# Performance work log

Hardware: AMD Instinct MI355X
Metric: run time of the kernel (lower is better)

## Reference

```python
import jax, jax.numpy as jnp
import numpy as np

N_NODES = 100000
N_EDGES = 1600000
B = 16
NMAX = 4096
IN_DIM = 32
H1 = 64      # capacity C
H2 = 128     # 2C
LAT = 64
DEC_H = 128  # 2C
DEC_IN = LAT + 2
FUEL = 5


def _ln(x, g, b):
    m = x.mean(-1, keepdims=True)
    v = x.var(-1, keepdims=True)
    return (x - m) / jnp.sqrt(v + 1e-5) * g + b


def _mlp2(x, wi, bi, g, be, wo, bo):
    # DeepMLP with num_layers=2: in_lin -> LayerNorm -> ReLU -> out_lin
    h = jax.nn.relu(_ln(x @ wi + bi, g, be))
    return h @ wo + bo


def setup_inputs() -> dict:
    key = jax.random.key(0)
    ks = jax.random.split(key, 48)
    d = {}
    d['x'] = jax.random.normal(ks[0], (N_NODES, IN_DIM), jnp.float32)
    d['edge_index'] = jax.random.randint(ks[1], (2, N_EDGES), 0, N_NODES)
    d['batch'] = jnp.sort(jax.random.randint(ks[2], (N_NODES,), 0, B))

    def w(k, shape):
        return (jax.random.normal(k, shape, jnp.float32) * 0.02)

    conv_shapes = {'w1m': (IN_DIM, H1), 'w2m': (H1, H2), 'w3m': (H2, LAT),
                   'w1l': (IN_DIM, H1), 'w2l': (H1, H2), 'w3l': (H2, LAT)}
    i = 3
    for nm, sh in conv_shapes.items():
        d[nm] = w(ks[i], sh); i += 1
        d['b' + nm[1:]] = jnp.zeros((sh[1],), jnp.float32)
    # node_mlp (DeepMLP dec_in->dec_h->dec_h)
    d['nm_wi'] = w(ks[i], (DEC_IN, DEC_H)); i += 1
    d['nm_bi'] = jnp.zeros((DEC_H,), jnp.float32)
    d['nm_g'] = jnp.ones((DEC_H,), jnp.float32)
    d['nm_be'] = jnp.zeros((DEC_H,), jnp.float32)
    d['nm_wo'] = w(ks[i], (DEC_H, DEC_H)); i += 1
    d['nm_bo'] = jnp.zeros((DEC_H,), jnp.float32)
    # heads
    d['ex_w'] = w(ks[i], (DEC_H, 1)); i += 1
    d['ex_b'] = jnp.zeros((1,), jnp.float32)
    d['fu_w'] = w(ks[i], (DEC_H, FUEL)); i += 1
    d['fu_b'] = jnp.zeros((FUEL,), jnp.float32)
    d['al_w'] = w(ks[i], (DEC_H, 1)); i += 1
    d['al_b'] = jnp.zeros((1,), jnp.float32)
    d['sl_w'] = w(ks[i], (DEC_H, 1)); i += 1
    d['sl_b'] = jnp.zeros((1,), jnp.float32)
    # edge_mlp (DeepMLP dec_in->dec_h->8)
    d['em_wi'] = w(ks[i], (DEC_IN, DEC_H)); i += 1
    d['em_bi'] = jnp.zeros((DEC_H,), jnp.float32)
    d['em_g'] = jnp.ones((DEC_H,), jnp.float32)
    d['em_be'] = jnp.zeros((DEC_H,), jnp.float32)
    d['em_wo'] = w(ks[i], (DEC_H, 8)); i += 1
    d['em_bo'] = jnp.zeros((8,), jnp.float32)
    d['pos_all'] = jax.random.normal(ks[i], (NMAX, 2), jnp.float32)
    return d


def reference(x, edge_index, batch,
              w1m, b1m, w2m, b2m, w3m, b3m,
              w1l, b1l, w2l, b2l, w3l, b3l,
              nm_wi, nm_bi, nm_g, nm_be, nm_wo, nm_bo,
              ex_w, ex_b, fu_w, fu_b, al_w, al_b, sl_w, sl_b,
              em_wi, em_bi, em_g, em_be, em_wo, em_bo,
              pos_all):
    # ---- GCN encoder with self-loops and symmetric normalization (PyG GCNConv) ----
    loops = jnp.arange(N_NODES)
    src = jnp.concatenate([edge_index[0], loops])
    dst = jnp.concatenate([edge_index[1], loops])
    deg = jax.ops.segment_sum(jnp.ones(src.shape, jnp.float32), dst, N_NODES)
    dinv = jax.lax.rsqrt(deg)  # deg >= 1 because of self-loops
    norm = (dinv[src] * dinv[dst])[:, None]

    def conv(h, wt, bt):
        hw = h @ wt                                   # [N, F_out]
        return jax.ops.segment_sum(norm * hw[src], dst, N_NODES) + bt

    mu = jax.nn.relu(conv(x, w1m, b1m))
    mu = jax.nn.relu(conv(mu, w2m, b2m))
    mu = jax.nn.relu(conv(mu, w3m, b3m))
    lg = jax.nn.relu(conv(x, w1l, b1l))
    lg = jax.nn.relu(conv(lg, w2l, b2l))
    lg = jax.nn.relu(conv(lg, w3l, b3l))

    cnt = jnp.maximum(jax.ops.segment_sum(jnp.ones((N_NODES,), jnp.float32), batch, B), 1.0)[:, None]
    mu_g = jax.ops.segment_sum(mu, batch, B) / cnt    # global_mean_pool [B, LAT]
    lg_g = jax.ops.segment_sum(lg, batch, B) / cnt

    z = mu_g  # eval-mode latent_sample returns mu

    # ---- decoder ----
    Z = jnp.broadcast_to(z[:, None, :], (B, NMAX, LAT))
    pos = jnp.broadcast_to(pos_all[None], (B, NMAX, 2))
    Zp = jnp.concatenate([Z, pos], -1).reshape(B * NMAX, DEC_IN)
    h = _mlp2(Zp, nm_wi, nm_bi, nm_g, nm_be, nm_wo, nm_bo)
    nodes = (h @ ex_w + ex_b).reshape(B, NMAX, 1)
    fuel = (h @ fu_w + fu_b).reshape(B, NMAX, FUEL)
    alt = (h @ al_w + al_b).reshape(B, NMAX, 1)
    slope = (h @ sl_w + sl_b).reshape(B, NMAX, 1)
    edges = _mlp2(Zp, em_wi, em_bi, em_g, em_be, em_wo, em_bo).reshape(B, NMAX, 8)
    return (nodes, edges, fuel, alt, slope, mu_g, lg_g)
```

## Files before the change

### kernel.cpp

```cpp
#include <hip/hip_runtime.h>
#include <hip/hip_bf16.h>

#define N_NODES 100000
#define N_EDGESC 1600000
#define BATCH_B 16
#define NMAXC 4096
#define LATC 64
#define NBINS 391
#define NSB 256
#define EPB ((N_EDGESC + NSB - 1) / NSB)
#define BIN_PAD 768

#define OUT_NODES 0
#define OUT_EDGES 65536
#define OUT_FUEL  589824
#define OUT_ALT   917504
#define OUT_SLOPE 983040
#define OUT_MU    1048576
#define OUT_LG    1049600

typedef float f32x2 __attribute__((ext_vector_type(2)));
typedef float f32x4 __attribute__((ext_vector_type(4)));
typedef short bf16x8 __attribute__((ext_vector_type(8)));
union U4B { uint4 u; bf16x8 b; };

__device__ __forceinline__ unsigned short f2bf(float f) {
    unsigned int u = __float_as_uint(f);
    return (unsigned short)((u + 0x7FFFu + ((u >> 16) & 1u)) >> 16);
}
__device__ __forceinline__ float bf2f(unsigned short h) {
    return __uint_as_float(((unsigned int)h) << 16);
}
__device__ __forceinline__ void f8acc(unsigned int u, float& a0, float& a1, float& a2, float& a3) {
    f32x2 lo = __builtin_amdgcn_cvt_pk_f32_fp8(u, false);
    f32x2 hi = __builtin_amdgcn_cvt_pk_f32_fp8(u, true);
    a0 += lo[0]; a1 += lo[1]; a2 += hi[0]; a3 += hi[1];
}
__device__ __forceinline__ void f8_to_bf2(unsigned int u, unsigned int& q0, unsigned int& q1) {
    f32x2 lo = __builtin_amdgcn_cvt_pk_f32_fp8(u, false);
    f32x2 hi = __builtin_amdgcn_cvt_pk_f32_fp8(u, true);
    q0 = (unsigned int)f2bf(lo[0]) | ((unsigned int)f2bf(lo[1]) << 16);
    q1 = (unsigned int)f2bf(hi[0]) | ((unsigned int)f2bf(hi[1]) << 16);
}

__global__ __launch_bounds__(1024) void histA(const int* __restrict__ dst, int* __restrict__ hist) {
    __shared__ int h[NBINS];
    int b = blockIdx.x, t = threadIdx.x;
    for (int i = t; i < NBINS; i += 1024) h[i] = 0;
    __syncthreads();
    int e0 = b * EPB, e1 = min(e0 + EPB, N_EDGESC);
    for (int i = e0 + t; i < e1; i += 1024)
        atomicAdd(&h[dst[i] >> 8], 1);
    __syncthreads();
    for (int i = t; i < NBINS; i += 1024) hist[i * NSB + b] = h[i];
}

__global__ void scanB(int* __restrict__ hist, int* __restrict__ total) {
    __shared__ int sh[NSB];
    int j = blockIdx.x, t = threadIdx.x;
    int v = hist[j * NSB + t];
    sh[t] = v; __syncthreads();
    for (int off = 1; off < NSB; off <<= 1) {
        int u = (t >= off) ? sh[t - off] : 0; __syncthreads();
        sh[t] += u; __syncthreads();
    }
    hist[j * NSB + t] = sh[t] - v;
    if (t == NSB - 1) total[j] = sh[t];
}

__global__ void scanC(const int* __restrict__ total, int* __restrict__ base) {
    __shared__ int sh[512];
    int t = threadIdx.x;
    int v = (t < NBINS) ? total[t] : 0;
    sh[t] = v; __syncthreads();
    for (int off = 1; off < 512; off <<= 1) {
        int u = (t >= off) ? sh[t - off] : 0; __syncthreads();
        sh[t] += u; __syncthreads();
    }
    if (t < NBINS) base[t] = sh[t] - v;
    if (t == NBINS - 1) base[NBINS] = sh[t];
}

__global__ __launch_bounds__(1024) void scatterD(const int* __restrict__ src, const int* __restrict__ dst,
                                                 const int* __restrict__ hist, const int* __restrict__ base,
                                                 unsigned int* __restrict__ sorted) {
    __shared__ int w0[NBINS];
    __shared__ int lc[NBINS];
    int b = blockIdx.x, t = threadIdx.x;
    for (int i = t; i < NBINS; i += 1024) {
        w0[i] = base[i] + hist[i * NSB + b];
        lc[i] = 0;
    }
    __syncthreads();
    int e0 = b * EPB, e1 = min(e0 + EPB, N_EDGESC);
    for (int i = e0 + t; i < e1; i += 1024) {
        int d = dst[i], s = src[i];
        int j = d >> 8;
        int r = atomicAdd(&lc[j], 1);
        sorted[w0[j] + r] = ((unsigned int)s << 8) | (d & 255);
    }
}

__global__ void csr_compact(const unsigned int* __restrict__ sorted, const int* __restrict__ base,
                            const float* __restrict__ x,
                            int* __restrict__ adj, int* __restrict__ offs,
                            int* __restrict__ cnt, float* __restrict__ dinv,
                            unsigned int* __restrict__ xs8, int N) {
    __shared__ int lc[256];
    __shared__ int cur[256];
    __shared__ int so4[256];
    int j = blockIdx.x, t = threadIdx.x;
    lc[t] = 0; cur[t] = 0;
    __syncthreads();
    int e0 = base[j], e1 = base[j + 1];
    for (int i = e0 + t; i < e1; i += 256)
        atomicAdd(&lc[sorted[i] & 255], 1);
    __syncthreads();
    int c4 = (lc[t] + 3) & ~3;
    so4[t] = c4;
    __syncthreads();
    for (int off = 1; off < 256; off <<= 1) {
        int u = (t >= off) ? so4[t - off] : 0; __syncthreads();
        so4[t] += u; __syncthreads();
    }
    int mybase = base[j] + j * BIN_PAD + so4[t] - c4;
    __syncthreads();
    so4[t] = mybase;
    __syncthreads();
    for (int i = e0 + t; i < e1; i += 256) {
        unsigned int pk = sorted[i];
        int d = pk & 255;
        int r = atomicAdd(&cur[d], 1);
        adj[so4[d] + r] = (int)(pk >> 8);
    }
    int n = j * 256 + t;
    if (n < N) {
        int c = lc[t];
        cnt[n] = c;
        offs[n] = so4[t];
        float dv = rsqrtf((float)(c + 1));
        dinv[n] = dv;
        float ds = dv * 64.f;
        const float* xr = &x[(size_t)n * 32];
        unsigned int q[8];
#pragma unroll
        for (int jj = 0; jj < 8; jj++) {
            float4 v = *(const float4*)&xr[jj * 4];
            unsigned int r8 = 0;
            r8 = __builtin_amdgcn_cvt_pk_fp8_f32(v.x * ds, v.y * ds, r8, false);
            r8 = __builtin_amdgcn_cvt_pk_fp8_f32(v.z * ds, v.w * ds, r8, true);
            q[jj] = r8;
        }
        *(uint4*)&xs8[(size_t)n * 8] = make_uint4(q[0], q[1], q[2], q[3]);
        *(uint4*)&xs8[(size_t)n * 8 + 4] = make_uint4(q[4], q[5], q[6], q[7]);
    }
}

__global__ void agg_s32(const unsigned int* __restrict__ xs8, const int* __restrict__ cnt,
                        const int* __restrict__ offs, const int* __restrict__ adj,
                        const float* __restrict__ dinv, unsigned short* __restrict__ outb, int N) {
    int t = threadIdx.x;
    int sub = t >> 3, f = t & 7;
    int n = blockIdx.x * 32 + sub;
    if (n >= N) return;
    float s0 = 0.f, s1 = 0.f, s2 = 0.f, s3 = 0.f;
    f8acc(xs8[(size_t)n * 8 + f], s0, s1, s2, s3);
    int e = offs[n];
    int e1 = e + cnt[n];
    for (; e + 8 <= e1; e += 8) {
        int4 ia = *(const int4*)&adj[e];
        int4 ib = *(const int4*)&adj[e + 4];
        unsigned int u0 = xs8[(size_t)ia.x * 8 + f];
        unsigned int u1 = xs8[(size_t)ia.y * 8 + f];
        unsigned int u2 = xs8[(size_t)ia.z * 8 + f];
        unsigned int u3 = xs8[(size_t)ia.w * 8 + f];
        unsigned int u4 = xs8[(size_t)ib.x * 8 + f];
        unsigned int u5 = xs8[(size_t)ib.y * 8 + f];
        unsigned int u6 = xs8[(size_t)ib.z * 8 + f];
        unsigned int u7 = xs8[(size_t)ib.w * 8 + f];
        f8acc(u0, s0, s1, s2, s3); f8acc(u1, s0, s1, s2, s3);
        f8acc(u2, s0, s1, s2, s3); f8acc(u3, s0, s1, s2, s3);
        f8acc(u4, s0, s1, s2, s3); f8acc(u5, s0, s1, s2, s3);
        f8acc(u6, s0, s1, s2, s3); f8acc(u7, s0, s1, s2, s3);
    }
    if (e + 4 <= e1) {
        int4 ia = *(const int4*)&adj[e];
        unsigned int u0 = xs8[(size_t)ia.x * 8 + f];
        unsigned int u1 = xs8[(size_t)ia.y * 8 + f];
        unsigned int u2 = xs8[(size_t)ia.z * 8 + f];
        unsigned int u3 = xs8[(size_t)ia.w * 8 + f];
        f8acc(u0, s0, s1, s2, s3); f8acc(u1, s0, s1, s2, s3);
        f8acc(u2, s0, s1, s2, s3); f8acc(u3, s0, s1, s2, s3);
        e += 4;
    }
    for (; e < e1; e++) f8acc(xs8[(size_t)adj[e] * 8 + f], s0, s1, s2, s3);
    float d = dinv[n] * (1.f / 64.f);
    ushort4 o;
    o.x = f2bf(s0 * d); o.y = f2bf(s1 * d); o.z = f2bf(s2 * d); o.w = f2bf(s3 * d);
    *(ushort4*)&outb[(size_t)n * 32 + f * 4] = o;
}

template <bool BIASRELU, bool OUT8>
__global__ void agg128(const unsigned int* __restrict__ tbl, const int* __restrict__ cnt,
                       const int* __restrict__ offs, const int* __restrict__ adj,
                       const float* __restrict__ dinv, const float* __restrict__ bias,
                       void* __restrict__ outv, int N) {
    int t = threadIdx.x;
    int sub = t >> 5, f = t & 31;
    int n = blockIdx.x * 8 + sub;
    if (n >= N) return;
    float s0 = 0.f, s1 = 0.f, s2 = 0.f, s3 = 0.f;
    f8acc(tbl[(size_t)n * 32 + f], s0, s1, s2, s3);
    int e = offs[n];
    int e1 = e + cnt[n];
    for (; e + 8 <= e1; e += 8) {
        int4 ia = *(const int4*)&adj[e];
        int4 ib = *(const int4*)&adj[e + 4];
        unsigned int u0 = tbl[(size_t)ia.x * 32 + f];
        unsigned int u1 = tbl[(size_t)ia.y * 32 + f];
        unsigned int u2 = tbl[(size_t)ia.z * 32 + f];
        unsigned int u3 = tbl[(size_t)ia.w * 32 + f];
        unsigned int u4 = tbl[(size_t)ib.x * 32 + f];
        unsigned int u5 = tbl[(size_t)ib.y * 32 + f];
        unsigned int u6 = tbl[(size_t)ib.z * 32 + f];
        unsigned int u7 = tbl[(size_t)ib.w * 32 + f];
        f8acc(u0, s0, s1, s2, s3); f8acc(u1, s0, s1, s2, s3);
        f8acc(u2, s0, s1, s2, s3); f8acc(u3, s0, s1, s2, s3);
        f8acc(u4, s0, s1, s2, s3); f8acc(u5, s0, s1, s2, s3);
        f8acc(u6, s0, s1, s2, s3); f8acc(u7, s0, s1, s2, s3);
    }
    if (e + 4 <= e1) {
        int4 ia = *(const int4*)&adj[e];
        unsigned int u0 = tbl[(size_t)ia.x * 32 + f];
        unsigned int u1 = tbl[(size_t)ia.y * 32 + f];
        unsigned int u2 = tbl[(size_t)ia.z * 32 + f];
        unsigned int u3 = tbl[(size_t)ia.w * 32 + f];
        f8acc(u0, s0, s1, s2, s3); f8acc(u1, s0, s1, s2, s3);
        f8acc(u2, s0, s1, s2, s3); f8acc(u3, s0, s1, s2, s3);
        e += 4;
    }
    for (; e < e1; e++) f8acc(tbl[(size_t)adj[e] * 32 + f], s0, s1, s2, s3);
    float d = dinv[n] * (1.f / 32.f);
    float v0 = s0 * d, v1 = s1 * d, v2 = s2 * d, v3 = s3 * d;
    if (BIASRELU) {
        float4 bv = *(const float4*)&bias[4 * f];
        v0 = fmaxf(v0 + bv.x, 0.f); v1 = fmaxf(v1 + bv.y, 0.f);
        v2 = fmaxf(v2 + bv.z, 0.f); v3 = fmaxf(v3 + bv.w, 0.f);
    }
    if (OUT8) {
        unsigned int r = 0;
        r = __builtin_amdgcn_cvt_pk_fp8_f32(v0 * 32.f, v1 * 32.f, r, false);
        r = __builtin_amdgcn_cvt_pk_fp8_f32(v2 * 32.f, v3 * 32.f, r, true);
        ((unsigned int*)outv)[(size_t)n * 32 + f] = r;
    } else {
        ushort4 u;
        u.x = f2bf(v0); u.y = f2bf(v1); u.z = f2bf(v2); u.w = f2bf(v3);
        *(ushort4*)&((unsigned short*)outv)[(size_t)n * 128 + 4 * f] = u;
    }
}

__device__ __forceinline__ void wfrag_write(const float* W, int F, int col, int k0,
                                            unsigned int* dst) {
    unsigned int q[4];
#pragma unroll
    for (int jj = 0; jj < 4; jj++) {
        float lo = W[(size_t)(k0 + 2 * jj) * F + col];
        float hi = W[(size_t)(k0 + 2 * jj + 1) * F + col];
        q[jj] = (unsigned int)f2bf(lo) | ((unsigned int)f2bf(hi) << 16);
    }
    *(uint4*)dst = make_uint4(q[0], q[1], q[2], q[3]);
}

__global__ void mega_prep(const int* __restrict__ batch,
                          const float* __restrict__ w1m, const float* __restrict__ w1l,
                          const float* __restrict__ b1m, const float* __restrict__ b1l,
                          const float* __restrict__ b3m, const float* __restrict__ b3l,
                          const float* __restrict__ w2m, const float* __restrict__ w2l,
                          const float* __restrict__ w3m, const float* __restrict__ w3l,
                          const float* __restrict__ nm_wo, const float* __restrict__ nm_bo,
                          const float* __restrict__ ex_w, const float* __restrict__ ex_b,
                          const float* __restrict__ fu_w, const float* __restrict__ fu_b,
                          const float* __restrict__ al_w, const float* __restrict__ al_b,
                          const float* __restrict__ sl_w, const float* __restrict__ sl_b,
                          const float* __restrict__ em_wo,
                          int* __restrict__ bcnt, float* __restrict__ bcat1,
                          float* __restrict__ bcat3, float* __restrict__ wtn,
                          float* __restrict__ bcn, float* __restrict__ wte,
                          unsigned int* __restrict__ wf1, unsigned int* __restrict__ wf2,
                          unsigned int* __restrict__ wf3) {
    int blk = blockIdx.x, t = threadIdx.x;
    if (blk == 0) {
        if (t < 128) bcat1[t] = (t < 64) ? b1m[t] : b1l[t - 64];
        else { int f = t - 128; bcat3[f] = (f < 64) ? b3m[f] : b3l[f - 64]; }
        if (t < BATCH_B) {
            int b = t;
            int lo = 0, hi = N_NODES;
            while (lo < hi) { int mid = (lo + hi) >> 1; if (batch[mid] < b) lo = mid + 1; else hi = mid; }
            int start = lo;
            lo = 0; hi = N_NODES;
            while (lo < hi) { int mid = (lo + hi) >> 1; if (batch[mid] <= b) lo = mid + 1; else hi = mid; }
            bcnt[b] = lo - start;
        }
    } else if (blk <= 9) {
        int idx = (blk - 1) * 256 + t;
        if (idx < 1024) {
            int j = idx >> 7, k = idx & 127;
            float s = 0.f;
            for (int m = 0; m < 128; m++) {
                float w = (j == 0) ? ex_w[m] : (j <= 5) ? fu_w[m * 5 + (j - 1)]
                         : (j == 6) ? al_w[m] : sl_w[m];
                s += nm_wo[k * 128 + m] * w;
            }
            wtn[j * 128 + k] = s;
        } else if (idx < 2048) {
            int i2 = idx - 1024;
            int j = i2 >> 7, k = i2 & 127;
            wte[j * 128 + k] = em_wo[k * 8 + j];
        } else if (idx < 2056) {
            int j = idx - 2048;
            float s = (j == 0) ? ex_b[0] : (j <= 5) ? fu_b[j - 1] : (j == 6) ? al_b[0] : sl_b[0];
            for (int m = 0; m < 128; m++) {
                float w = (j == 0) ? ex_w[m] : (j <= 5) ? fu_w[m * 5 + (j - 1)]
                         : (j == 6) ? al_w[m] : sl_w[m];
                s += nm_bo[m] * w;
            }
            bcn[j] = s;
        }
    } else if (blk <= 17) {
        if (t < 64) {
            int c = blk - 10;
            int col = c * 16 + (t & 15);
            int k0 = (t >> 4) * 8;
            unsigned int q[4];
#pragma unroll
            for (int jj = 0; jj < 4; jj++) {
                int ka = k0 + 2 * jj, kb = ka + 1;
                float lo = (col < 64) ? w1m[ka * 64 + col] : w1l[ka * 64 + col - 64];
                float hi = (col < 64) ? w1m[kb * 64 + col] : w1l[kb * 64 + col - 64];
                q[jj] = (unsigned int)f2bf(lo) | ((unsigned int)f2bf(hi) << 16);
            }
            *(uint4*)&wf1[((size_t)c * 64 + t) * 4] = make_uint4(q[0], q[1], q[2], q[3]);
        }
    } else if (blk <= 49) {
        if (t < 64) {
            int bc = blk - 18;
            int c = bc % 8, s = (bc / 8) % 2, y = bc / 16;
            const float* W = y ? w2l : w2m;
            wfrag_write(W, 128, c * 16 + (t & 15), s * 32 + (t >> 4) * 8,
                        &wf2[((size_t)bc * 64 + t) * 4]);
        }
    } else {
        if (t < 64) {
            int bc = blk - 50;
            int c = bc % 4, s = (bc / 4) % 4, y = bc / 16;
            const float* W = y ? w3l : w3m;
            wfrag_write(W, 64, c * 16 + (t & 15), s * 32 + (t >> 4) * 8,
                        &wf3[((size_t)bc * 64 + t) * 4]);
        }
    }
}

__global__ __launch_bounds__(256) void mfma_conv1(
    const unsigned short* __restrict__ inv, const unsigned int* __restrict__ wfrag,
    const float* __restrict__ bias, const float* __restrict__ dinv,
    unsigned int* __restrict__ outv, int N) {
    constexpr int C = 8;
    constexpr int FP = 132;
    __shared__ unsigned short buf[4][16][FP];
    int t = threadIdx.x, lane = t & 63, wave = t >> 6;
    int n0 = blockIdx.x * 64 + wave * 16;

    f32x4 acc[C];
#pragma unroll
    for (int c = 0; c < C; c++) acc[c] = (f32x4)(0.f);

    int arow = n0 + (lane & 15);
    bool aok = arow < N;
    U4B af; af.u = make_uint4(0u, 0u, 0u, 0u);
    if (aok)
        af.u = *(const uint4*)(inv + (size_t)arow * 32 + (lane >> 4) * 8);
#pragma unroll
    for (int c = 0; c < C; c++) {
        U4B wb;
        wb.u = *(const uint4*)&wfrag[((size_t)c * 64 + lane) * 4];
        acc[c] = __builtin_amdgcn_mfma_f32_16x16x32_bf16(af.b, wb.b, acc[c], 0, 0, 0);
    }

#pragma unroll
    for (int c = 0; c < C; c++) {
        int col = c * 16 + (lane & 15);
        float bv = bias[col];
#pragma unroll
        for (int r = 0; r < 4; r++) {
            int row = (lane >> 4) * 4 + r;
            int n = n0 + row;
            float v = fmaxf(acc[c][r] + bv, 0.f) * dinv[min(n, N - 1)];
            buf[wave][row][col] = f2bf(v);
        }
    }
    __syncthreads();

    for (int i = t; i < 64 * 16; i += 256) {
        int row = i / 16;
        int f0 = (i % 16) * 8;
        int n = blockIdx.x * 64 + row;
        if (n >= N) continue;
        const unsigned short* bp = &buf[row >> 4][row & 15][f0];
        uint2 a = *(const uint2*)bp;
        uint2 b = *(const uint2*)(bp + 4);
        float e0 = __uint_as_float(a.x << 16), e1 = __uint_as_float(a.x & 0xFFFF0000u);
        float e2 = __uint_as_float(a.y << 16), e3 = __uint_as_float(a.y & 0xFFFF0000u);
        float e4 = __uint_as_float(b.x << 16), e5 = __uint_as_float(b.x & 0xFFFF0000u);
        float e6 = __uint_as_float(b.y << 16), e7 = __uint_as_float(b.y & 0xFFFF0000u);
        unsigned int r0 = 0, r1 = 0;
        r0 = __builtin_amdgcn_cvt_pk_fp8_f32(e0 * 32.f, e1 * 32.f, r0, false);
        r0 = __builtin_amdgcn_cvt_pk_fp8_f32(e2 * 32.f, e3 * 32.f, r0, true);
        r1 = __builtin_amdgcn_cvt_pk_fp8_f32(e4 * 32.f, e5 * 32.f, r1, false);
        r1 = __builtin_amdgcn_cvt_pk_fp8_f32(e6 * 32.f, e7 * 32.f, r1, true);
        *(uint2*)((unsigned char*)outv + (size_t)n * 128 + f0) = make_uint2(r0, r1);
    }
}

__global__ __launch_bounds__(256) void conv23(
    const unsigned int* __restrict__ hB8, const unsigned int* __restrict__ wf2,
    const unsigned int* __restrict__ wf3, const float* __restrict__ b2m,
    const float* __restrict__ b2l, const float* __restrict__ dinv,
    unsigned int* __restrict__ hD8, int N) {
    __shared__ unsigned short hbuf[4][16][136];
    __shared__ unsigned short obuf[4][16][72];
    int t = threadIdx.x, lane = t & 63, wave = t >> 6;
    int y = blockIdx.y;
    int n0 = blockIdx.x * 64 + wave * 16;
    const float* bias = y ? b2l : b2m;
    const unsigned int* w2 = wf2 + (size_t)y * 2 * 8 * 64 * 4;
    const unsigned int* w3 = wf3 + (size_t)y * 4 * 4 * 64 * 4;

    f32x4 acc2[8];
#pragma unroll
    for (int c = 0; c < 8; c++) acc2[c] = (f32x4)(0.f);
    int arow = n0 + (lane & 15);
    bool aok = arow < N;
#pragma unroll
    for (int s = 0; s < 2; s++) {
        U4B af; af.u = make_uint4(0u, 0u, 0u, 0u);
        if (aok) {
            uint2 u = *(const uint2*)((const unsigned char*)hB8 +
                        (size_t)arow * 128 + y * 64 + s * 32 + (lane >> 4) * 8);
            f8_to_bf2(u.x, af.u.x, af.u.y);
            f8_to_bf2(u.y, af.u.z, af.u.w);
        }
#pragma unroll
        for (int c = 0; c < 8; c++) {
            U4B wb;
            wb.u = *(const uint4*)&w2[((size_t)(s * 8 + c) * 64 + lane) * 4];
            acc2[c] = __builtin_amdgcn_mfma_f32_16x16x32_bf16(af.b, wb.b, acc2[c], 0, 0, 0);
        }
    }
#pragma unroll
    for (int c = 0; c < 8; c++) {
        int col = c * 16 + (lane & 15);
        float bv = bias[col];
#pragma unroll
        for (int r = 0; r < 4; r++) {
            int row = (lane >> 4) * 4 + r;
            float v = fmaxf(acc2[c][r] * (1.f / 32.f) + bv, 0.f);
            hbuf[wave][row][col] = f2bf(v);
        }
    }

    f32x4 acc3[4];
#pragma unroll
    for (int c = 0; c < 4; c++) acc3[c] = (f32x4)(0.f);
#pragma unroll
    for (int s = 0; s < 4; s++) {
        U4B af;
        af.u = *(const uint4*)&hbuf[wave][lane & 15][s * 32 + (lane >> 4) * 8];
#pragma unroll
        for (int c = 0; c < 4; c++) {
            U4B wb;
            wb.u = *(const uint4*)&w3[((size_t)(s * 4 + c) * 64 + lane) * 4];
            acc3[c] = __builtin_amdgcn_mfma_f32_16x16x32_bf16(af.b, wb.b, acc3[c], 0, 0, 0);
        }
    }
#pragma unroll
    for (int c = 0; c < 4; c++) {
        int col = c * 16 + (lane & 15);
#pragma unroll
        for (int r = 0; r < 4; r++) {
            int row = (lane >> 4) * 4 + r;
            int n = n0 + row;
            float v = acc3[c][r] * dinv[min(n, N - 1)];
            obuf[wave][row][col] = f2bf(v);
        }
    }
    __syncthreads();
    for (int i = t; i < 64 * 8; i += 256) {
        int row = i / 8;
        int f0 = (i % 8) * 8;
        int n = blockIdx.x * 64 + row;
        if (n >= N) continue;
        const unsigned short* bp = &obuf[row >> 4][row & 15][f0];
        uint2 a = *(const uint2*)bp;
        uint2 b = *(const uint2*)(bp + 4);
        float e0 = __uint_as_float(a.x << 16), e1 = __uint_as_float(a.x & 0xFFFF0000u);
        float e2 = __uint_as_float(a.y << 16), e3 = __uint_as_float(a.y & 0xFFFF0000u);
        float e4 = __uint_as_float(b.x << 16), e5 = __uint_as_float(b.x & 0xFFFF0000u);
        float e6 = __uint_as_float(b.y << 16), e7 = __uint_as_float(b.y & 0xFFFF0000u);
        unsigned int r0 = 0, r1 = 0;
        r0 = __builtin_amdgcn_cvt_pk_fp8_f32(e0 * 32.f, e1 * 32.f, r0, false);
        r0 = __builtin_amdgcn_cvt_pk_fp8_f32(e2 * 32.f, e3 * 32.f, r0, true);
        r1 = __builtin_amdgcn_cvt_pk_fp8_f32(e4 * 32.f, e5 * 32.f, r1, false);
        r1 = __builtin_amdgcn_cvt_pk_fp8_f32(e6 * 32.f, e7 * 32.f, r1, true);
        *(uint2*)((unsigned char*)hD8 + (size_t)n * 128 + y * 64 + f0) = make_uint2(r0, r1);
    }
}

__global__ __launch_bounds__(256) void pool128(const unsigned int* __restrict__ h,
                                               const int* __restrict__ batch,
                                               float* __restrict__ sums, int n) {
    int t = threadIdx.x, lane = t & 63, wave = t >> 6;
    int r0 = blockIdx.x * 64 + wave * 16;
    if (r0 >= n) return;
    int r1 = min(r0 + 16, n);
    int cur = batch[r0];
    float a0 = 0.f, a1 = 0.f;
    for (int i = r0; i < r1; i++) {
        int b = batch[i];
        if (b != cur) {
            atomicAdd(&sums[cur * 128 + 2 * lane], a0);
            atomicAdd(&sums[cur * 128 + 2 * lane + 1], a1);
            a0 = a1 = 0.f; cur = b;
        }
        unsigned int u = h[(size_t)i * 64 + lane];
        a0 += __uint_as_float(u << 16);
        a1 += __uint_as_float(u & 0xFFFF0000u);
    }
    atomicAdd(&sums[cur * 128 + 2 * lane], a0);
    atomicAdd(&sums[cur * 128 + 2 * lane + 1], a1);
}

__global__ void finalize_zwi(const float* __restrict__ sums, const int* __restrict__ bcnt,
                             const float* __restrict__ nm_wi, const float* __restrict__ nm_bi,
                             const float* __restrict__ em_wi, const float* __restrict__ em_bi,
                             float* __restrict__ out, float* __restrict__ zwi_nm,
                             float* __restrict__ zwi_em) {
    __shared__ float zs[64];
    int b = blockIdx.x, t = threadIdx.x;
    float c = fmaxf((float)bcnt[b], 1.f);
    float v = sums[b * 128 + t] / c;
    if (t < 64) { out[OUT_MU + b * 64 + t] = v; zs[t] = v; }
    else out[OUT_LG + b * 64 + (t - 64)] = v;
    __syncthreads();
    float an = nm_bi[t], ae = em_bi[t];
    for (int k = 0; k < 64; k++) {
        float zv = zs[k];
        an += zv * nm_wi[k * 128 + t];
        ae += zv * em_wi[k * 128 + t];
    }
    zwi_nm[b * 128 + t] = an;
    zwi_em[b * 128 + t] = ae;
}

#define D3_ROWS 32

__global__ __launch_bounds__(256) void decoder3(
    const float* __restrict__ zwi_nm, const float* __restrict__ zwi_em,
    const float* __restrict__ nm_wi, const float* __restrict__ em_wi,
    const float* __restrict__ nm_g, const float* __restrict__ nm_be,
    const float* __restrict__ em_g, const float* __restrict__ em_be,
    const float* __restrict__ wtn, const float* __restrict__ bcn,
    const float* __restrict__ wte, const float* __restrict__ em_bo,
    const float* __restrict__ pos_all,
    float* __restrict__ out) {
    __shared__ float sn[D3_ROWS][132];
    __shared__ float se[D3_ROWS][132];
    __shared__ float Wn[8][132];
    __shared__ float We[8][132];
    int t = threadIdx.x;
    int lane = t & 63, wave = t >> 6;
    int rowBase = blockIdx.x * D3_ROWS;
    int b = rowBase >> 12;
    int row0 = rowBase + wave * 8;

    for (int i = t; i < 1024; i += 256) {
        Wn[i >> 7][i & 127] = wtn[i];
        We[i >> 7][i & 127] = wte[i];
    }

    int f0 = lane, f1 = lane + 64;
    float zn0 = zwi_nm[b * 128 + f0], zn1 = zwi_nm[b * 128 + f1];
    float ze0 = zwi_em[b * 128 + f0], ze1 = zwi_em[b * 128 + f1];
    float wn64_0 = nm_wi[64 * 128 + f0], wn64_1 = nm_wi[64 * 128 + f1];
    float wn65_0 = nm_wi[65 * 128 + f0], wn65_1 = nm_wi[65 * 128 + f1];
    float we64_0 = em_wi[64 * 128 + f0], we64_1 = em_wi[64 * 128 + f1];
    float we65_0 = em_wi[65 * 128 + f0], we65_1 = em_wi[65 * 128 + f1];
    float gn0 = nm_g[f0], gn1 = nm_g[f1], bn0 = nm_be[f0], bn1 = nm_be[f1];
    float ge0 = em_g[f0], ge1 = em_g[f1], be0 = em_be[f0], be1 = em_be[f1];

#pragma unroll
    for (int r = 0; r < 8; r++) {
        int row = row0 + r, i = row & (NMAXC - 1);
        float px = pos_all[i * 2], py = pos_all[i * 2 + 1];
        float a0 = zn0 + px * wn64_0 + py * wn65_0;
        float a1 = zn1 + px * wn64_1 + py * wn65_1;
        float e0 = ze0 + px * we64_0 + py * we65_0;
        float e1 = ze1 + px * we64_1 + py * we65_1;
        float sm = a0 + a1, sq = a0 * a0 + a1 * a1;
        float sme = e0 + e1, sqe = e0 * e0 + e1 * e1;
#pragma unroll
        for (int d = 1; d < 64; d <<= 1) {
            sm += __shfl_xor(sm, d); sq += __shfl_xor(sq, d);
            sme += __shfl_xor(sme, d); sqe += __shfl_xor(sqe, d);
        }
        float mean = sm * (1.f / 128.f);
        float var = sq * (1.f / 128.f) - mean * mean;
        float rstd = rsqrtf(var + 1e-5f);
        int rl = wave * 8 + r;
        sn[rl][f0] = fmaxf((a0 - mean) * rstd * gn0 + bn0, 0.f);
        sn[rl][f1] = fmaxf((a1 - mean) * rstd * gn1 + bn1, 0.f);
        float meane = sme * (1.f / 128.f);
        float vare = sqe * (1.f / 128.f) - meane * meane;
        float rstde = rsqrtf(vare + 1e-5f);
        se[rl][f0] = fmaxf((e0 - meane) * rstde * ge0 + be0, 0.f);
        se[rl][f1] = fmaxf((e1 - meane) * rstde * ge1 + be1, 0.f);
    }
    __syncthreads();

    int rl = t >> 3, j = t & 7;
    float accn = 0.f, acce = 0.f;
#pragma unroll 8
    for (int k4 = 0; k4 < 128; k4 += 4) {
        float4 sv = *(const float4*)&sn[rl][k4];
        float4 wv = *(const float4*)&Wn[j][k4];
        float4 sev = *(const float4*)&se[rl][k4];
        float4 wev = *(const float4*)&We[j][k4];
        accn += sv.x * wv.x + sv.y * wv.y + sv.z * wv.z + sv.w * wv.w;
        acce += sev.x * wev.x + sev.y * wev.y + sev.z * wev.z + sev.w * wev.w;
    }
    int row = rowBase + rl;
    accn += bcn[j];
    if (j == 0)       out[OUT_NODES + row] = accn;
    else if (j <= 5)  out[OUT_FUEL + (size_t)row * 5 + (j - 1)] = accn;
    else if (j == 6)  out[OUT_ALT + row] = accn;
    else              out[OUT_SLOPE + row] = accn;
    out[OUT_EDGES + (size_t)row * 8 + j] = acce + em_bo[j];
}

extern "C" void kernel_launch(void* const* d_in, const int* in_sizes, int n_in,
                              void* d_out, int out_size, void* d_ws, size_t ws_size,
                              hipStream_t stream) {
    const float* x    = (const float*)d_in[0];
    const int* edge   = (const int*)d_in[1];
    const int* batch  = (const int*)d_in[2];
    const float* w1m = (const float*)d_in[3];  const float* b1m = (const float*)d_in[4];
    const float* w2m = (const float*)d_in[5];  const float* b2m = (const float*)d_in[6];
    const float* w3m = (const float*)d_in[7];  const float* b3m = (const float*)d_in[8];
    const float* w1l = (const float*)d_in[9];  const float* b1l = (const float*)d_in[10];
    const float* w2l = (const float*)d_in[11]; const float* b2l = (const float*)d_in[12];
    const float* w3l = (const float*)d_in[13]; const float* b3l = (const float*)d_in[14];
    const float* nm_wi = (const float*)d_in[15]; const float* nm_bi = (const float*)d_in[16];
    const float* nm_g  = (const float*)d_in[17]; const float* nm_be = (const float*)d_in[18];
    const float* nm_wo = (const float*)d_in[19]; const float* nm_bo = (const float*)d_in[20];
    const float* ex_w = (const float*)d_in[21]; const float* ex_b = (const float*)d_in[22];
    const float* fu_w = (const float*)d_in[23]; const float* fu_b = (const float*)d_in[24];
    const float* al_w = (const float*)d_in[25]; const float* al_b = (const float*)d_in[26];
    const float* sl_w = (const float*)d_in[27]; const float* sl_b = (const float*)d_in[28];
    const float* em_wi = (const float*)d_in[29]; const float* em_bi = (const float*)d_in[30];
    const float* em_g  = (const float*)d_in[31]; const float* em_be = (const float*)d_in[32];
    const float* em_wo = (const float*)d_in[33]; const float* em_bo = (const float*)d_in[34];
    const float* pos_all = (const float*)d_in[35];
    float* out = (float*)d_out;

    char* p = (char*)d_ws;
    auto alloc = [&](size_t bytes) -> void* {
        void* r = (void*)p;
        p += ((bytes + 255) / 256) * 256;
        return r;
    };
    int* cnt      = (int*)alloc((size_t)N_NODES * 4);
    int* offs     = (int*)alloc((size_t)N_NODES * 4);
    float* dinv   = (float*)alloc((size_t)N_NODES * 4);
    int* bcnt     = (int*)alloc(BATCH_B * 4);
    float* sums   = (float*)alloc(BATCH_B * 128 * 4);
    float* zwi_nm = (float*)alloc(BATCH_B * 128 * 4);
    float* zwi_em = (float*)alloc(BATCH_B * 128 * 4);
    float* bcat1  = (float*)alloc(128 * 4);
    float* bcat3  = (float*)alloc(128 * 4);
    float* wtn    = (float*)alloc(8 * 128 * 4);
    float* bcn    = (float*)alloc(8 * 4);
    float* wte    = (float*)alloc(8 * 128 * 4);
    unsigned int* wf1 = (unsigned int*)alloc((size_t)8 * 64 * 4 * 4);
    unsigned int* wf2 = (unsigned int*)alloc((size_t)32 * 64 * 4 * 4);
    unsigned int* wf3 = (unsigned int*)alloc((size_t)32 * 64 * 4 * 4);
    int* hist     = (int*)alloc((size_t)NBINS * NSB * 4);
    int* total    = (int*)alloc((size_t)NBINS * 4);
    int* base     = (int*)alloc((size_t)(NBINS + 1) * 4);
    unsigned int* sorted = (unsigned int*)alloc((size_t)N_EDGESC * 4);
    int* adj      = (int*)alloc((size_t)(N_EDGESC + NBINS * BIN_PAD + 256) * 4);
    unsigned int* xs8 = (unsigned int*)alloc((size_t)N_NODES * 8 * 4);
    unsigned short* agg0b = (unsigned short*)alloc((size_t)N_NODES * 32 * 2);
    unsigned int* hA8 = (unsigned int*)alloc((size_t)N_NODES * 32 * 4);
    unsigned int* hB8 = (unsigned int*)alloc((size_t)N_NODES * 32 * 4);
    unsigned short* final128 = (unsigned short*)alloc((size_t)N_NODES * 128 * 2);
    unsigned int* hD8 = hA8;

    const int* srcp = edge;
    const int* dstp = edge + N_EDGESC;

    hipMemsetAsync(sums, 0, (size_t)BATCH_B * 128 * 4, stream);

    mega_prep<<<82, 256, 0, stream>>>(batch, w1m, w1l, b1m, b1l, b3m, b3l,
                                      w2m, w2l, w3m, w3l, nm_wo, nm_bo,
                                      ex_w, ex_b, fu_w, fu_b, al_w, al_b, sl_w, sl_b,
                                      em_wo, bcnt, bcat1, bcat3, wtn, bcn, wte,
                                      wf1, wf2, wf3);

    histA<<<NSB, 1024, 0, stream>>>(dstp, hist);
    scanB<<<NBINS, NSB, 0, stream>>>(hist, total);
    scanC<<<1, 512, 0, stream>>>(total, base);
    scatterD<<<NSB, 1024, 0, stream>>>(srcp, dstp, hist, base, sorted);
    csr_compact<<<NBINS, 256, 0, stream>>>(sorted, base, x, adj, offs, cnt, dinv, xs8, N_NODES);

    agg_s32<<<(N_NODES + 31) / 32, 256, 0, stream>>>(xs8, cnt, offs, adj, dinv, agg0b, N_NODES);

    const int GB = (N_NODES + 63) / 64;

    mfma_conv1<<<GB, 256, 0, stream>>>(agg0b, wf1, bcat1, dinv, hA8, N_NODES);

    agg128<false, true><<<(N_NODES + 7) / 8, 256, 0, stream>>>(
        hA8, cnt, offs, adj, dinv, nullptr, hB8, N_NODES);

    conv23<<<dim3(GB, 2), 256, 0, stream>>>(hB8, wf2, wf3, b2m, b2l, dinv, hD8, N_NODES);

    agg128<true, false><<<(N_NODES + 7) / 8, 256, 0, stream>>>(
        hD8, cnt, offs, adj, dinv, bcat3, final128, N_NODES);

    pool128<<<GB, 256, 0, stream>>>((const unsigned int*)final128, batch, sums, N_NODES);
    finalize_zwi<<<BATCH_B, 128, 0, stream>>>(sums, bcnt, nm_wi, nm_bi, em_wi, em_bi,
                                              out, zwi_nm, zwi_em);

    decoder3<<<BATCH_B * NMAXC / D3_ROWS, 256, 0, stream>>>(
        zwi_nm, zwi_em, nm_wi, em_wi, nm_g, nm_be, em_g, em_be,
        wtn, bcn, wte, em_bo, pos_all, out);
}
```

Before: 259.4 us.

## Slice 128-wide fp8 feature tables into XCD-affine 32-feature planes for aggregation

Stores the fp8 hidden tables as four planar slices of 32 features per node instead of interleaved 128-byte rows. Each aggregation block is mapped, via blockIdx modulo 8, so that a pair of XCDs handles one feature slice, so each XCD's L2 only needs to cache a quarter of the gather table. Producers (conv1, conv23) and the consumer conv23 read are updated for the new layout. The cost is that each thread now gathers 4 bytes from 8 lanes per row, so row reads are shorter, and adjacency and offsets are re-read four times.

```diff
diff --git a/kernel.cpp b/kernel.cpp
--- a/kernel.cpp
+++ b/kernel.cpp
@@ -201,29 +201,34 @@
 }
 
 template <bool BIASRELU, bool OUT8>
-__global__ void agg128(const unsigned int* __restrict__ tbl, const int* __restrict__ cnt,
-                       const int* __restrict__ offs, const int* __restrict__ adj,
-                       const float* __restrict__ dinv, const float* __restrict__ bias,
-                       void* __restrict__ outv, int N) {
+__global__ __launch_bounds__(256) void agg128s(
+    const unsigned int* __restrict__ tbl, const int* __restrict__ cnt,
+    const int* __restrict__ offs, const int* __restrict__ adj,
+    const float* __restrict__ dinv, const float* __restrict__ bias,
+    void* __restrict__ outv, int N) {
     int t = threadIdx.x;
-    int sub = t >> 5, f = t & 31;
-    int n = blockIdx.x * 8 + sub;
+    int sub = t >> 3, f = t & 7;
+    int xcd = blockIdx.x & 7;
+    int slice = xcd >> 1;
+    int chunk = (blockIdx.x >> 3) * 2 + (xcd & 1);
+    int n = chunk * 32 + sub;
     if (n >= N) return;
+    const unsigned int* ts = tbl + (size_t)slice * N * 8;
     float s0 = 0.f, s1 = 0.f, s2 = 0.f, s3 = 0.f;
-    f8acc(tbl[(size_t)n * 32 + f], s0, s1, s2, s3);
+    f8acc(ts[(size_t)n * 8 + f], s0, s1, s2, s3);
     int e = offs[n];
     int e1 = e + cnt[n];
     for (; e + 8 <= e1; e += 8) {
         int4 ia = *(const int4*)&adj[e];
         int4 ib = *(const int4*)&adj[e + 4];
-        unsigned int u0 = tbl[(size_t)ia.x * 32 + f];
-        unsigned int u1 = tbl[(size_t)ia.y * 32 + f];
-        unsigned int u2 = tbl[(size_t)ia.z * 32 + f];
-        unsigned int u3 = tbl[(size_t)ia.w * 32 + f];
-        unsigned int u4 = tbl[(size_t)ib.x * 32 + f];
-        unsigned int u5 = tbl[(size_t)ib.y * 32 + f];
-        unsigned int u6 = tbl[(size_t)ib.z * 32 + f];
-        unsigned int u7 = tbl[(size_t)ib.w * 32 + f];
+        unsigned int u0 = ts[(size_t)ia.x * 8 + f];
+        unsigned int u1 = ts[(size_t)ia.y * 8 + f];
+        unsigned int u2 = ts[(size_t)ia.z * 8 + f];
+        unsigned int u3 = ts[(size_t)ia.w * 8 + f];
+        unsigned int u4 = ts[(size_t)ib.x * 8 + f];
+        unsigned int u5 = ts[(size_t)ib.y * 8 + f];
+        unsigned int u6 = ts[(size_t)ib.z * 8 + f];
+        unsigned int u7 = ts[(size_t)ib.w * 8 + f];
         f8acc(u0, s0, s1, s2, s3); f8acc(u1, s0, s1, s2, s3);
         f8acc(u2, s0, s1, s2, s3); f8acc(u3, s0, s1, s2, s3);
         f8acc(u4, s0, s1, s2, s3); f8acc(u5, s0, s1, s2, s3);
@@ -231,19 +236,19 @@
     }
     if (e + 4 <= e1) {
         int4 ia = *(const int4*)&adj[e];
-        unsigned int u0 = tbl[(size_t)ia.x * 32 + f];
-        unsigned int u1 = tbl[(size_t)ia.y * 32 + f];
-        unsigned int u2 = tbl[(size_t)ia.z * 32 + f];
-        unsigned int u3 = tbl[(size_t)ia.w * 32 + f];
+        unsigned int u0 = ts[(size_t)ia.x * 8 + f];
+        unsigned int u1 = ts[(size_t)ia.y * 8 + f];
+        unsigned int u2 = ts[(size_t)ia.z * 8 + f];
+        unsigned int u3 = ts[(size_t)ia.w * 8 + f];
         f8acc(u0, s0, s1, s2, s3); f8acc(u1, s0, s1, s2, s3);
         f8acc(u2, s0, s1, s2, s3); f8acc(u3, s0, s1, s2, s3);
         e += 4;
     }
-    for (; e < e1; e++) f8acc(tbl[(size_t)adj[e] * 32 + f], s0, s1, s2, s3);
+    for (; e < e1; e++) f8acc(ts[(size_t)adj[e] * 8 + f], s0, s1, s2, s3);
     float d = dinv[n] * (1.f / 32.f);
     float v0 = s0 * d, v1 = s1 * d, v2 = s2 * d, v3 = s3 * d;
     if (BIASRELU) {
-        float4 bv = *(const float4*)&bias[4 * f];
+        float4 bv = ((const float4*)bias)[slice * 8 + f];
         v0 = fmaxf(v0 + bv.x, 0.f); v1 = fmaxf(v1 + bv.y, 0.f);
         v2 = fmaxf(v2 + bv.z, 0.f); v3 = fmaxf(v3 + bv.w, 0.f);
     }
@@ -251,11 +256,11 @@
         unsigned int r = 0;
         r = __builtin_amdgcn_cvt_pk_fp8_f32(v0 * 32.f, v1 * 32.f, r, false);
         r = __builtin_amdgcn_cvt_pk_fp8_f32(v2 * 32.f, v3 * 32.f, r, true);
-        ((unsigned int*)outv)[(size_t)n * 32 + f] = r;
+        ((unsigned int*)outv)[((size_t)slice * N + n) * 8 + f] = r;
     } else {
         ushort4 u;
         u.x = f2bf(v0); u.y = f2bf(v1); u.z = f2bf(v2); u.w = f2bf(v3);
-        *(ushort4*)&((unsigned short*)outv)[(size_t)n * 128 + 4 * f] = u;
+        *(ushort4*)&((unsigned short*)outv)[(size_t)n * 128 + slice * 32 + f * 4] = u;
     }
 }
 
@@ -417,7 +422,8 @@
         r0 = __builtin_amdgcn_cvt_pk_fp8_f32(e2 * 32.f, e3 * 32.f, r0, true);
         r1 = __builtin_amdgcn_cvt_pk_fp8_f32(e4 * 32.f, e5 * 32.f, r1, false);
         r1 = __builtin_amdgcn_cvt_pk_fp8_f32(e6 * 32.f, e7 * 32.f, r1, true);
-        *(uint2*)((unsigned char*)outv + (size_t)n * 128 + f0) = make_uint2(r0, r1);
+        *(uint2*)((unsigned char*)outv + ((size_t)(f0 >> 5) * N + n) * 32 + (f0 & 31))
+            = make_uint2(r0, r1);
     }
 }
 
@@ -445,7 +451,7 @@
         U4B af; af.u = make_uint4(0u, 0u, 0u, 0u);
         if (aok) {
             uint2 u = *(const uint2*)((const unsigned char*)hB8 +
-                        (size_t)arow * 128 + y * 64 + s * 32 + (lane >> 4) * 8);
+                        ((size_t)(y * 2 + s) * N + arow) * 32 + (lane >> 4) * 8);
             f8_to_bf2(u.x, af.u.x, af.u.y);
             f8_to_bf2(u.y, af.u.z, af.u.w);
         }
@@ -511,7 +517,9 @@
         r0 = __builtin_amdgcn_cvt_pk_fp8_f32(e2 * 32.f, e3 * 32.f, r0, true);
         r1 = __builtin_amdgcn_cvt_pk_fp8_f32(e4 * 32.f, e5 * 32.f, r1, false);
         r1 = __builtin_amdgcn_cvt_pk_fp8_f32(e6 * 32.f, e7 * 32.f, r1, true);
-        *(uint2*)((unsigned char*)hD8 + (size_t)n * 128 + y * 64 + f0) = make_uint2(r0, r1);
+        int F = y * 64 + f0;
+        *(uint2*)((unsigned char*)hD8 + ((size_t)(F >> 5) * N + n) * 32 + (F & 31))
+            = make_uint2(r0, r1);
     }
 }
 
@@ -724,15 +732,17 @@
     agg_s32<<<(N_NODES + 31) / 32, 256, 0, stream>>>(xs8, cnt, offs, adj, dinv, agg0b, N_NODES);
 
     const int GB = (N_NODES + 63) / 64;
+    const int NCHUNK = (N_NODES + 31) / 32;
+    const int AGG_GRID = ((NCHUNK + 1) / 2) * 8;
 
     mfma_conv1<<<GB, 256, 0, stream>>>(agg0b, wf1, bcat1, dinv, hA8, N_NODES);
 
-    agg128<false, true><<<(N_NODES + 7) / 8, 256, 0, stream>>>(
+    agg128s<false, true><<<AGG_GRID, 256, 0, stream>>>(
         hA8, cnt, offs, adj, dinv, nullptr, hB8, N_NODES);
 
     conv23<<<dim3(GB, 2), 256, 0, stream>>>(hB8, wf2, wf3, b2m, b2l, dinv, hD8, N_NODES);
 
-    agg128<true, false><<<(N_NODES + 7) / 8, 256, 0, stream>>>(
+    agg128s<true, false><<<AGG_GRID, 256, 0, stream>>>(
         hD8, cnt, offs, adj, dinv, bcat3, final128, N_NODES);
 
     pool128<<<GB, 256, 0, stream>>>((const unsigned int*)final128, batch, sums, N_NODES);
```

Measured after the change: 277.9 us. 7.1% more time.
